# Performance work log

Hardware: AMD Instinct MI355X
Metric: run time of the kernel (lower is better)

Reference implementation:

```python
import jax, jax.numpy as jnp
import numpy as np
import math

SAMPLING_FACTOR = 5


def setup_inputs() -> dict:
    key = jax.random.key(0)
    kq, kk, kv, ki = jax.random.split(key, 4)
    B, L_Q, L_K, d = 8, 4096, 4096, 64
    # U_part = min(5 * L_Q * ceil(log1p(L_K)), L_K) = 4096 for these sizes
    U_part = min(SAMPLING_FACTOR * L_Q * math.ceil(math.log1p(L_K)), L_K)
    q = jax.random.normal(kq, (B, L_Q, d), dtype=jnp.float32)
    K = jax.random.normal(kk, (B, L_K, d), dtype=jnp.float32)
    V = jax.random.normal(kv, (B, L_K, d), dtype=jnp.float32)
    index_sample = jax.random.randint(ki, (U_part,), 0, L_K)  # random key sample (torch.randint)
    return {"q": q, "K": K, "V": V, "index_sample": index_sample}


def reference(q, K, V, index_sample):
    B, L_Q, d = q.shape
    L_K = K.shape[1]
    log_L_Q = math.ceil(math.log1p(L_Q))
    u = min(SAMPLING_FACTOR * log_L_Q, L_Q)  # number of selected queries (45 here)

    # Random key sampling (indices shared across batch)
    K_sample = K[:, index_sample, :]                       # [B, U_part, d]
    # Q @ K_sample^T
    Q_K_sample = jnp.einsum('bqd,bud->bqu', q, K_sample)   # [B, L_Q, U_part]
    # Sparsity measure M = max - sum/L_K
    M = Q_K_sample.max(axis=-1) - Q_K_sample.sum(axis=-1) / L_K  # [B, L_Q]
    # Source uses topk(..., largest=False): pick queries with SMALLEST M (kept faithfully)
    _, M_top = jax.lax.top_k(-M, u)                        # [B, u]
    # Gather the selected queries
    Q_reduce = jnp.take_along_axis(q, M_top[:, :, None], axis=1)  # [B, u, d]
    # Full attention over all keys for the selected queries
    attn_scores = jnp.einsum('bud,bkd->buk', Q_reduce, K) / math.sqrt(d)  # [B, u, L_K]
    attn_probs = jax.nn.softmax(attn_scores, axis=-1)
    attn_output = jnp.einsum('buk,bkd->bud', attn_probs, V)  # [B, u, d]
    return attn_output, attn_scores
```

## Files before the change

kernel.cpp:

```cpp
#include <hip/hip_runtime.h>
#include <hip/hip_bf16.h>
#include <math.h>

#define BB 8
#define LQ 4096
#define LK 4096
#define DD 64
#define UU 45
#define CCAP 256
#define CUMTHR 96
#define ECH 32

typedef __bf16 bf16x8 __attribute__((ext_vector_type(8)));
typedef unsigned short ushort8 __attribute__((ext_vector_type(8)));
typedef float f32x4 __attribute__((ext_vector_type(4)));

__device__ inline unsigned short f2bf(float x) {
    unsigned u = __builtin_bit_cast(unsigned, x);
    return (unsigned short)((u + 0x7FFF + ((u >> 16) & 1)) >> 16);
}

__device__ inline void gl_lds16(const void* g, void* l) {
    __builtin_amdgcn_global_load_lds(
        (const __attribute__((address_space(1))) unsigned int*)g,
        (__attribute__((address_space(3))) unsigned int*)l, 16, 0, 0);
}

__global__ __launch_bounds__(256) void k_gatherK(const float* __restrict__ K,
                                                 const int* __restrict__ idx,
                                                 int Upart,
                                                 unsigned short* __restrict__ Kg,
                                                 double* __restrict__ part) {
    int b = blockIdx.y;
    int chunk = blockIdx.x;
    int u0 = chunk * 256;
    int t = threadIdx.x;
    int pt = t & 7;

    double acc[8] = {0,0,0,0,0,0,0,0};
    #pragma unroll
    for (int i = 0; i < 8; ++i) {
        int lin = i * 256 + t;
        int u = u0 + (lin >> 3);
        if (u < Upart) {
            int kr = idx[u];
            const float* src = &K[((size_t)b * LK + kr) * DD + pt * 8];
            float4 v0 = *(const float4*)src;
            float4 v1 = *(const float4*)(src + 4);
            ushort8 pk;
            pk[0]=f2bf(v0.x); pk[1]=f2bf(v0.y); pk[2]=f2bf(v0.z); pk[3]=f2bf(v0.w);
            pk[4]=f2bf(v1.x); pk[5]=f2bf(v1.y); pk[6]=f2bf(v1.z); pk[7]=f2bf(v1.w);
            *(ushort8*)&Kg[((size_t)b * 4096 + u) * 64 + pt * 8] = pk;
            acc[0] += (double)v0.x; acc[1] += (double)v0.y;
            acc[2] += (double)v0.z; acc[3] += (double)v0.w;
            acc[4] += (double)v1.x; acc[5] += (double)v1.y;
            acc[6] += (double)v1.z; acc[7] += (double)v1.w;
        }
    }
    __shared__ double sred[32][64];
    int rg = t >> 3;
    #pragma unroll
    for (int j = 0; j < 8; ++j) sred[rg][pt * 8 + j] = acc[j];
    __syncthreads();
    if (t < 64) {
        double s = 0.0;
        #pragma unroll
        for (int r = 0; r < 32; ++r) s += sred[r][t];
        part[((size_t)(b * 16 + chunk)) * 64 + t] = s;
    }
}

__global__ __launch_bounds__(64) void k_sumK_red(const double* __restrict__ part,
                                                 int nch, double* __restrict__ sumK) {
    int b = blockIdx.x;
    int d = threadIdx.x;
    double s = 0.0;
    for (int ch = 0; ch < nch; ++ch)
        s += part[((size_t)(b * 16 + ch)) * 64 + d];
    sumK[b * DD + d] = s;
}

__global__ __launch_bounds__(256) void k_mfmaM(const float* __restrict__ Q,
                                               const unsigned short* __restrict__ Kg,
                                               float* __restrict__ maxpart) {
    int bx = blockIdx.x, cg = blockIdx.y, b = blockIdx.z;
    int t = threadIdx.x;
    int lane = t & 63, w = t >> 6;
    int row0 = bx * 128;

    __shared__ unsigned short Qs[128 * 64];
    __shared__ unsigned short Ks[2][128 * 64];

    for (int i = 0; i < 4; ++i) {
        int u = i * 256 + t;
        int r = u >> 3, s = u & 7;
        int c = s ^ (r & 7);
        const float* src = &Q[((size_t)b * LQ + row0 + r) * DD + c * 8];
        float4 v0 = *(const float4*)src;
        float4 v1 = *(const float4*)(src + 4);
        ushort8 pk;
        pk[0]=f2bf(v0.x); pk[1]=f2bf(v0.y); pk[2]=f2bf(v0.z); pk[3]=f2bf(v0.w);
        pk[4]=f2bf(v1.x); pk[5]=f2bf(v1.y); pk[6]=f2bf(v1.z); pk[7]=f2bf(v1.w);
        *(ushort8*)&Qs[r * 64 + s * 8] = pk;
    }

    int krl = lane >> 3;
    int kc8 = (lane & 7) ^ (krl & 7);
    const unsigned short* kgb = Kg + ((size_t)b * 4096 + cg * 2048) * 64;

    #define STAGE_K(buf, tile)                                                  \
        {                                                                       \
            _Pragma("unroll")                                                   \
            for (int i_ = 0; i_ < 4; ++i_) {                                    \
                int seg_ = w * 4 + i_;                                          \
                const unsigned short* g_ =                                      \
                    kgb + ((size_t)((tile) * 128 + seg_ * 8 + krl)) * 64 + kc8 * 8; \
                gl_lds16(g_, &Ks[buf][seg_ * 512]);                             \
            }                                                                   \
        }

    STAGE_K(0, 0)
    __syncthreads();

    bf16x8 afr[2][2];
    #pragma unroll
    for (int rf = 0; rf < 2; ++rf)
        #pragma unroll
        for (int kh = 0; kh < 2; ++kh) {
            int r = w * 32 + rf * 16 + (lane & 15);
            int slot = (kh * 4 + (lane >> 4)) ^ (r & 7);
            afr[rf][kh] = __builtin_bit_cast(bf16x8, *(const ushort8*)&Qs[r * 64 + slot * 8]);
        }

    float rowmax[2][4];
    #pragma unroll
    for (int rf = 0; rf < 2; ++rf)
        #pragma unroll
        for (int g = 0; g < 4; ++g) rowmax[rf][g] = -INFINITY;

    for (int tile = 0; tile < 16; ++tile) {
        int cur = tile & 1;
        if (tile < 15) STAGE_K(cur ^ 1, tile + 1)

        #pragma unroll
        for (int cf = 0; cf < 8; ++cf) {
            f32x4 acc0 = {0.f, 0.f, 0.f, 0.f};
            f32x4 acc1 = {0.f, 0.f, 0.f, 0.f};
            #pragma unroll
            for (int kh = 0; kh < 2; ++kh) {
                int ccol = cf * 16 + (lane & 15);
                int slot = (kh * 4 + (lane >> 4)) ^ (ccol & 7);
                bf16x8 bfr = __builtin_bit_cast(bf16x8, *(const ushort8*)&Ks[cur][ccol * 64 + slot * 8]);
                acc0 = __builtin_amdgcn_mfma_f32_16x16x32_bf16(afr[0][kh], bfr, acc0, 0, 0, 0);
                acc1 = __builtin_amdgcn_mfma_f32_16x16x32_bf16(afr[1][kh], bfr, acc1, 0, 0, 0);
            }
            #pragma unroll
            for (int g = 0; g < 4; ++g) {
                rowmax[0][g] = fmaxf(rowmax[0][g], acc0[g]);
                rowmax[1][g] = fmaxf(rowmax[1][g], acc1[g]);
            }
        }
        __syncthreads();
    }

    #pragma unroll
    for (int rf = 0; rf < 2; ++rf)
        #pragma unroll
        for (int g = 0; g < 4; ++g) {
            float m = rowmax[rf][g];
            m = fmaxf(m, __shfl_xor(m, 1));
            m = fmaxf(m, __shfl_xor(m, 2));
            m = fmaxf(m, __shfl_xor(m, 4));
            m = fmaxf(m, __shfl_xor(m, 8));
            if ((lane & 15) == 0) {
                int row = row0 + w * 32 + rf * 16 + (lane >> 4) * 4 + g;
                maxpart[((size_t)(b * 2 + cg)) * LQ + row] = m;
            }
        }
}

__global__ __launch_bounds__(256) void k_meanmerge(const float* __restrict__ Q,
                                                   const double* __restrict__ sumK,
                                                   const float* __restrict__ maxpart,
                                                   double* __restrict__ mt,
                                                   float* __restrict__ Map) {
    int b = blockIdx.y;
    int r = blockIdx.x * 256 + threadIdx.x;
    const float* qr = &Q[((size_t)b * LQ + r) * DD];
    const double* s = &sumK[b * DD];
    double a0 = 0, a1 = 0, a2 = 0, a3 = 0;
    #pragma unroll
    for (int d = 0; d < 64; d += 4) {
        a0 += (double)qr[d + 0] * s[d + 0];
        a1 += (double)qr[d + 1] * s[d + 1];
        a2 += (double)qr[d + 2] * s[d + 2];
        a3 += (double)qr[d + 3] * s[d + 3];
    }
    double m = ((a0 + a1) + (a2 + a3)) / (double)LK;
    mt[(size_t)b * LQ + r] = m;
    float mx = fmaxf(maxpart[((size_t)(b * 2 + 0)) * LQ + r],
                     maxpart[((size_t)(b * 2 + 1)) * LQ + r]);
    Map[(size_t)b * LQ + r] = mx - (float)m;
}

__global__ __launch_bounds__(256) void k_select(const float* __restrict__ Map,
                                                int* __restrict__ cand,
                                                int* __restrict__ cand_count) {
    int b = blockIdx.x;
    int t = threadIdx.x;
    __shared__ float mv[LQ];
    __shared__ int hist[1024];
    __shared__ float wmin[4], wmax[4];
    __shared__ float s_min, s_max;
    __shared__ int s_bstar, s_cnt;

    float lmin = INFINITY, lmax = -INFINITY;
    for (int i = t; i < LQ; i += 256) {
        float v = Map[(size_t)b * LQ + i];
        mv[i] = v;
        lmin = fminf(lmin, v);
        lmax = fmaxf(lmax, v);
    }
    #pragma unroll
    for (int m = 1; m < 64; m <<= 1) {
        lmin = fminf(lmin, __shfl_xor(lmin, m));
        lmax = fmaxf(lmax, __shfl_xor(lmax, m));
    }
    int wid = t >> 6;
    if ((t & 63) == 0) { wmin[wid] = lmin; wmax[wid] = lmax; }
    for (int i = t; i < 1024; i += 256) hist[i] = 0;
    __syncthreads();
    if (t == 0) {
        s_min = fminf(fminf(wmin[0], wmin[1]), fminf(wmin[2], wmin[3]));
        s_max = fmaxf(fmaxf(wmax[0], wmax[1]), fmaxf(wmax[2], wmax[3]));
        s_cnt = 0;
    }
    __syncthreads();
    float vmin = s_min;
    float w = (s_max - vmin) * (1.0f / 1024.0f);
    if (w <= 0.f) w = 1e-30f;
    float inv = 1.0f / w;
    for (int i = t; i < LQ; i += 256) {
        int bin = (int)((mv[i] - vmin) * inv);
        bin = min(max(bin, 0), 1023);
        atomicAdd(&hist[bin], 1);
    }
    __syncthreads();
    if (t == 0) {
        int cum = 0, bs = 1023;
        for (int j = 0; j < 1024; ++j) {
            cum += hist[j];
            if (cum >= CUMTHR) { bs = j; break; }
        }
        s_bstar = bs;
    }
    __syncthreads();
    int bstar = s_bstar;
    for (int i = t; i < LQ; i += 256) {
        int bin = (int)((mv[i] - vmin) * inv);
        bin = min(max(bin, 0), 1023);
        if (bin <= bstar) {
            int p = atomicAdd(&s_cnt, 1);
            if (p < CCAP) cand[b * CCAP + p] = i;
        }
    }
    __syncthreads();
    if (t == 0) cand_count[b] = min(s_cnt, CCAP);
}

__global__ __launch_bounds__(256, 1) void k_exact(const float* __restrict__ Q,
                                                  const float* __restrict__ K,
                                                  const int* __restrict__ idx,
                                                  const int* __restrict__ cand,
                                                  const int* __restrict__ cand_count,
                                                  float* __restrict__ exactpart) {
    int kc = blockIdx.x;
    int b  = blockIdx.y;
    int t = threadIdx.x;
    int lane = t & 63, w = t >> 6;
    __shared__ float Ks[128 * 64];
    __shared__ float wmx[4][CCAP];

    #pragma unroll
    for (int p = 0; p < 8; ++p) {
        int row = p * 16 + (t >> 4);
        int c4 = t & 15;
        int kr = idx[kc * 128 + row];
        *(float4*)&Ks[row * 64 + c4 * 4] =
            *(const float4*)&K[((size_t)b * LK + kr) * DD + c4 * 4];
    }

    int count = cand_count[b];
    int npass = (count + 127) >> 7;
    __syncthreads();

    for (int pass = 0; pass < npass; ++pass) {
        int s0 = pass * 128 + lane;
        int s1 = s0 + 64;
        float4 q0[16], q1[16];
        {
            float4 z = {0.f, 0.f, 0.f, 0.f};
            if (s0 < count) {
                const float4* qp = (const float4*)&Q[((size_t)b * LQ + cand[b * CCAP + s0]) * DD];
                #pragma unroll
                for (int i = 0; i < 16; ++i) q0[i] = qp[i];
            } else {
                #pragma unroll
                for (int i = 0; i < 16; ++i) q0[i] = z;
            }
            if (s1 < count) {
                const float4* qp = (const float4*)&Q[((size_t)b * LQ + cand[b * CCAP + s1]) * DD];
                #pragma unroll
                for (int i = 0; i < 16; ++i) q1[i] = qp[i];
            } else {
                #pragma unroll
                for (int i = 0; i < 16; ++i) q1[i] = z;
            }
        }

        float m0 = -INFINITY, m1 = -INFINITY;
        int kbeg = w * 32;
        for (int k = kbeg; k < kbeg + 32; ++k) {
            const float4* kr4 = (const float4*)&Ks[k * 64];
            float a0=0.f,a1=0.f,a2=0.f,a3=0.f;
            float c0=0.f,c1=0.f,c2=0.f,c3=0.f;
            #pragma unroll
            for (int i = 0; i < 16; i += 4) {
                float4 kv0 = kr4[i+0], kv1 = kr4[i+1], kv2 = kr4[i+2], kv3 = kr4[i+3];
                a0 = fmaf(q0[i+0].x, kv0.x, a0); a0 = fmaf(q0[i+0].y, kv0.y, a0);
                a0 = fmaf(q0[i+0].z, kv0.z, a0); a0 = fmaf(q0[i+0].w, kv0.w, a0);
                a1 = fmaf(q0[i+1].x, kv1.x, a1); a1 = fmaf(q0[i+1].y, kv1.y, a1);
                a1 = fmaf(q0[i+1].z, kv1.z, a1); a1 = fmaf(q0[i+1].w, kv1.w, a1);
                a2 = fmaf(q0[i+2].x, kv2.x, a2); a2 = fmaf(q0[i+2].y, kv2.y, a2);
                a2 = fmaf(q0[i+2].z, kv2.z, a2); a2 = fmaf(q0[i+2].w, kv2.w, a2);
                a3 = fmaf(q0[i+3].x, kv3.x, a3); a3 = fmaf(q0[i+3].y, kv3.y, a3);
                a3 = fmaf(q0[i+3].z, kv3.z, a3); a3 = fmaf(q0[i+3].w, kv3.w, a3);
                c0 = fmaf(q1[i+0].x, kv0.x, c0); c0 = fmaf(q1[i+0].y, kv0.y, c0);
                c0 = fmaf(q1[i+0].z, kv0.z, c0); c0 = fmaf(q1[i+0].w, kv0.w, c0);
                c1 = fmaf(q1[i+1].x, kv1.x, c1); c1 = fmaf(q1[i+1].y, kv1.y, c1);
                c1 = fmaf(q1[i+1].z, kv1.z, c1); c1 = fmaf(q1[i+1].w, kv1.w, c1);
                c2 = fmaf(q1[i+2].x, kv2.x, c2); c2 = fmaf(q1[i+2].y, kv2.y, c2);
                c2 = fmaf(q1[i+2].z, kv2.z, c2); c2 = fmaf(q1[i+2].w, kv2.w, c2);
                c3 = fmaf(q1[i+3].x, kv3.x, c3); c3 = fmaf(q1[i+3].y, kv3.y, c3);
                c3 = fmaf(q1[i+3].z, kv3.z, c3); c3 = fmaf(q1[i+3].w, kv3.w, c3);
            }
            m0 = fmaxf(m0, (a0 + a1) + (a2 + a3));
            m1 = fmaxf(m1, (c0 + c1) + (c2 + c3));
        }
        wmx[w][s0] = m0;
        if (s1 < CCAP) wmx[w][s1] = m1;
    }
    __syncthreads();

    if (t < count) {
        float m = fmaxf(fmaxf(wmx[0][t], wmx[1][t]), fmaxf(wmx[2][t], wmx[3][t]));
        exactpart[((size_t)(b * CCAP + t)) * ECH + kc] = m;
    }
}

__global__ __launch_bounds__(64) void k_final45(const float* __restrict__ exactpart,
                                                const double* __restrict__ mt,
                                                const int* __restrict__ cand,
                                                const int* __restrict__ cand_count,
                                                int* __restrict__ Mtop) {
    int b = blockIdx.x;
    int l = threadIdx.x;
    int count = cand_count[b];
    float val[4];
    int oid[4];
    #pragma unroll
    for (int j = 0; j < 4; ++j) {
        int slot = l + j * 64;
        if (slot < count) {
            const float* ep = &exactpart[((size_t)(b * CCAP + slot)) * ECH];
            float m = ep[0];
            #pragma unroll
            for (int k = 1; k < ECH; ++k) m = fmaxf(m, ep[k]);
            int r = cand[b * CCAP + slot];
            val[j] = m - (float)mt[(size_t)b * LQ + r];
            oid[j] = r;
        } else { val[j] = INFINITY; oid[j] = 0x7FFFFFFF; }
    }
    for (int it = 0; it < UU; ++it) {
        float bv = val[0]; int bi = oid[0], bj = 0;
        #pragma unroll
        for (int j = 1; j < 4; ++j)
            if (val[j] < bv || (val[j] == bv && oid[j] < bi)) { bv = val[j]; bi = oid[j]; bj = j; }
        float rv = bv; int ri = bi;
        #pragma unroll
        for (int m = 1; m < 64; m <<= 1) {
            float ov = __shfl_xor(rv, m);
            int oi = __shfl_xor(ri, m);
            if (ov < rv || (ov == rv && oi < ri)) { rv = ov; ri = oi; }
        }
        if (l == 0) Mtop[b * UU + it] = ri;
        if (rv == bv && ri == bi) val[bj] = INFINITY;
    }
}

__global__ __launch_bounds__(256) void k_scores(const float* __restrict__ Q,
                                                const float* __restrict__ K,
                                                const int* __restrict__ Mtop,
                                                float* __restrict__ scores) {
    int ch = blockIdx.x, b = blockIdx.y;
    int t = threadIdx.x;
    __shared__ float Qs[UU][64];
    for (int i = t; i < UU * 64; i += 256) {
        int r = i >> 6, dd = i & 63;
        int qrow = Mtop[b * UU + r];
        Qs[r][dd] = Q[((size_t)b * LQ + qrow) * DD + dd];
    }
    __syncthreads();

    int k = ch * 256 + t;
    const float* Krow = &K[((size_t)b * LK + k) * DD];
    float acc[UU];
    #pragma unroll
    for (int r = 0; r < UU; ++r) acc[r] = 0.f;

    #pragma unroll 4
    for (int dq = 0; dq < 16; ++dq) {
        float4 kv = *(const float4*)&Krow[dq * 4];
        #pragma unroll
        for (int r = 0; r < UU; ++r) {
            float4 qv = *(const float4*)&Qs[r][dq * 4];
            acc[r] += qv.x * kv.x + qv.y * kv.y + qv.z * kv.z + qv.w * kv.w;
        }
    }
    #pragma unroll
    for (int r = 0; r < UU; ++r)
        scores[((size_t)(b * UU + r)) * LK + k] = acc[r] * 0.125f;
}

__global__ __launch_bounds__(256) void k_smstats(const float* __restrict__ scores,
                                                 float2* __restrict__ ms) {
    int r = blockIdx.x, b = blockIdx.y;
    int t = threadIdx.x;
    const float* row = &scores[((size_t)(b * UU + r)) * LK];
    float v[16];
    float m = -INFINITY;
    #pragma unroll
    for (int i = 0; i < 16; ++i) { v[i] = row[t + 256 * i]; m = fmaxf(m, v[i]); }
    #pragma unroll
    for (int off = 32; off; off >>= 1) m = fmaxf(m, __shfl_xor(m, off));
    __shared__ float wred[4];
    int wid = t >> 6, lane = t & 63;
    if (lane == 0) wred[wid] = m;
    __syncthreads();
    m = fmaxf(fmaxf(wred[0], wred[1]), fmaxf(wred[2], wred[3]));
    __syncthreads();
    float s = 0.f;
    #pragma unroll
    for (int i = 0; i < 16; ++i) s += __expf(v[i] - m);
    #pragma unroll
    for (int off = 32; off; off >>= 1) s += __shfl_xor(s, off);
    if (lane == 0) wred[wid] = s;
    __syncthreads();
    if (t == 0) ms[b * UU + r] = make_float2(m, wred[0] + wred[1] + wred[2] + wred[3]);
}

__global__ __launch_bounds__(256) void k_pv(const float* __restrict__ scores,
                                            const float2* __restrict__ ms,
                                            const float* __restrict__ V,
                                            float* __restrict__ partial) {
    int ch = blockIdx.x, b = blockIdx.y;
    int t = threadIdx.x;
    int k0 = ch * 128;
    __shared__ float Vs[128 * 64];
    __shared__ float Ps[48 * 128];

    for (int p = 0; p < 8; ++p) {
        int lin = p * 1024 + t * 4;
        *(float4*)&Vs[lin] = *(const float4*)&V[((size_t)b * LK + k0) * DD + lin];
    }
    for (int i = t; i < 48 * 128; i += 256) {
        int r = i >> 7, kk = i & 127;
        float p = 0.f;
        if (r < UU) {
            float2 m_s = ms[b * UU + r];
            float sc = scores[((size_t)(b * UU + r)) * LK + k0 + kk];
            p = __expf(sc - m_s.x) / m_s.y;
        }
        Ps[i] = p;
    }
    __syncthreads();

    int d = t & 63, rg = t >> 6;
    float acc[12];
    #pragma unroll
    for (int i = 0; i < 12; ++i) acc[i] = 0.f;
    for (int k = 0; k < 128; ++k) {
        float vv = Vs[k * 64 + d];
        #pragma unroll
        for (int i = 0; i < 12; ++i)
            acc[i] += Ps[(rg * 12 + i) * 128 + k] * vv;
    }
    #pragma unroll
    for (int i = 0; i < 12; ++i) {
        int r = rg * 12 + i;
        if (r < UU)
            partial[(((size_t)(b * 32 + ch)) * UU + r) * 64 + d] = acc[i];
    }
}

__global__ __launch_bounds__(256) void k_reduce(const float* __restrict__ partial,
                                                float* __restrict__ out) {
    int o = blockIdx.x * 256 + threadIdx.x;
    if (o >= BB * UU * 64) return;
    int b = o / (UU * 64);
    int rd = o % (UU * 64);
    float s = 0.f;
    for (int ch = 0; ch < 32; ++ch)
        s += partial[(((size_t)(b * 32 + ch)) * UU * 64) + rd];
    out[o] = s;
}

extern "C" void kernel_launch(void* const* d_in, const int* in_sizes, int n_in,
                              void* d_out, int out_size, void* d_ws, size_t ws_size,
                              hipStream_t stream) {
    const float* q   = (const float*)d_in[0];
    const float* K   = (const float*)d_in[1];
    const float* V   = (const float*)d_in[2];
    const int*   idx = (const int*)d_in[3];
    int Upart = in_sizes[3];
    int nch = (Upart + 255) / 256;

    char* ws = (char*)d_ws;
    size_t off = 0;
    unsigned short* Kg = (unsigned short*)(ws + off); off += (size_t)BB * 4096 * 64 * 2;
    double* sumK      = (double*)(ws + off); off += (size_t)BB * 64 * 8;
    float*  maxpart   = (float*)(ws + off);  off += (size_t)BB * 2 * LQ * 4;
    double* mt        = (double*)(ws + off); off += (size_t)BB * LQ * 8;
    float*  Map       = (float*)(ws + off);  off += (size_t)BB * LQ * 4;
    int*    cand      = (int*)(ws + off);    off += (size_t)BB * CCAP * 4;
    int*    cand_cnt  = (int*)(ws + off);    off += 256;
    int*    Mtop      = (int*)(ws + off);    off += 2048;
    float2* ms        = (float2*)(ws + off); off += 4096;
    float*  partial   = (float*)(ws + off);  off += (size_t)BB * 32 * UU * 64 * 4;
    double* sumKpart  = (double*)partial;
    float*  exactpart = (float*)partial;

    float* out_attn   = (float*)d_out;
    float* out_scores = out_attn + BB * UU * 64;

    k_gatherK  <<<dim3(nch, BB), 256, 0, stream>>>(K, idx, Upart, Kg, sumKpart);
    k_sumK_red <<<dim3(BB), 64, 0, stream>>>(sumKpart, nch, sumK);
    k_mfmaM    <<<dim3(LQ / 128, 2, BB), 256, 0, stream>>>(q, Kg, maxpart);
    k_meanmerge<<<dim3(LQ / 256, BB), 256, 0, stream>>>(q, sumK, maxpart, mt, Map);
    k_select   <<<dim3(BB), 256, 0, stream>>>(Map, cand, cand_cnt);
    k_exact    <<<dim3(ECH, BB), 256, 0, stream>>>(q, K, idx, cand, cand_cnt, exactpart);
    k_final45  <<<dim3(BB), 64, 0, stream>>>(exactpart, mt, cand, cand_cnt, Mtop);
    k_scores   <<<dim3(LK / 256, BB), 256, 0, stream>>>(q, K, Mtop, out_scores);
    k_smstats  <<<dim3(UU, BB), 256, 0, stream>>>(out_scores, ms);
    k_pv       <<<dim3(LK / 128, BB), 256, 0, stream>>>(out_scores, ms, V, partial);
    k_reduce   <<<dim3((BB * UU * 64 + 255) / 256), 256, 0, stream>>>(partial, out_attn);
}
```

Before: 165.0 us.

## Fuse scores, softmax and PV into split-K flash-style kernel with combine

Replaces the separate scores, softmax-stats, PV and reduce kernels with one kernel that computes a 128-key chunk of scores, does a local softmax, multiplies by V, and emits per-chunk max/sum stats. A combine kernel then rescales and merges the partial results. It also folds the sumK reduction into meanmerge and replaces the serial histogram scan in select with a parallel prefix scan. The intent is to cut kernel launches and the re-reads of the scores array, in exchange for only 32 blocks per batch in the fused kernel and an extra rescale step.

```diff
diff --git a/kernel.cpp b/kernel.cpp
--- a/kernel.cpp
+++ b/kernel.cpp
@@ -10,6 +10,7 @@
 #define CCAP 256
 #define CUMTHR 96
 #define ECH 32
+#define PCH 32
 
 typedef __bf16 bf16x8 __attribute__((ext_vector_type(8)));
 typedef unsigned short ushort8 __attribute__((ext_vector_type(8)));
@@ -70,16 +71,6 @@
     }
 }
 
-__global__ __launch_bounds__(64) void k_sumK_red(const double* __restrict__ part,
-                                                 int nch, double* __restrict__ sumK) {
-    int b = blockIdx.x;
-    int d = threadIdx.x;
-    double s = 0.0;
-    for (int ch = 0; ch < nch; ++ch)
-        s += part[((size_t)(b * 16 + ch)) * 64 + d];
-    sumK[b * DD + d] = s;
-}
-
 __global__ __launch_bounds__(256) void k_mfmaM(const float* __restrict__ Q,
                                                const unsigned short* __restrict__ Kg,
                                                float* __restrict__ maxpart) {
@@ -180,21 +171,30 @@
 }
 
 __global__ __launch_bounds__(256) void k_meanmerge(const float* __restrict__ Q,
-                                                   const double* __restrict__ sumK,
+                                                   const double* __restrict__ part,
+                                                   int nch,
                                                    const float* __restrict__ maxpart,
                                                    double* __restrict__ mt,
                                                    float* __restrict__ Map) {
     int b = blockIdx.y;
-    int r = blockIdx.x * 256 + threadIdx.x;
+    int t = threadIdx.x;
+    int r = blockIdx.x * 256 + t;
+    __shared__ double sK[64];
+    if (t < 64) {
+        double s = 0.0;
+        for (int ch = 0; ch < nch; ++ch)
+            s += part[((size_t)(b * 16 + ch)) * 64 + t];
+        sK[t] = s;
+    }
+    __syncthreads();
     const float* qr = &Q[((size_t)b * LQ + r) * DD];
-    const double* s = &sumK[b * DD];
     double a0 = 0, a1 = 0, a2 = 0, a3 = 0;
     #pragma unroll
     for (int d = 0; d < 64; d += 4) {
-        a0 += (double)qr[d + 0] * s[d + 0];
-        a1 += (double)qr[d + 1] * s[d + 1];
-        a2 += (double)qr[d + 2] * s[d + 2];
-        a3 += (double)qr[d + 3] * s[d + 3];
+        a0 += (double)qr[d + 0] * sK[d + 0];
+        a1 += (double)qr[d + 1] * sK[d + 1];
+        a2 += (double)qr[d + 2] * sK[d + 2];
+        a3 += (double)qr[d + 3] * sK[d + 3];
     }
     double m = ((a0 + a1) + (a2 + a3)) / (double)LK;
     mt[(size_t)b * LQ + r] = m;
@@ -210,6 +210,7 @@
     int t = threadIdx.x;
     __shared__ float mv[LQ];
     __shared__ int hist[1024];
+    __shared__ int seg[256];
     __shared__ float wmin[4], wmax[4];
     __shared__ float s_min, s_max;
     __shared__ int s_bstar, s_cnt;
@@ -234,6 +235,7 @@
         s_min = fminf(fminf(wmin[0], wmin[1]), fminf(wmin[2], wmin[3]));
         s_max = fmaxf(fmaxf(wmax[0], wmax[1]), fmaxf(wmax[2], wmax[3]));
         s_cnt = 0;
+        s_bstar = 1023;
     }
     __syncthreads();
     float vmin = s_min;
@@ -246,13 +248,26 @@
         atomicAdd(&hist[bin], 1);
     }
     __syncthreads();
-    if (t == 0) {
-        int cum = 0, bs = 1023;
-        for (int j = 0; j < 1024; ++j) {
-            cum += hist[j];
-            if (cum >= CUMTHR) { bs = j; break; }
-        }
-        s_bstar = bs;
+    int h0 = hist[t * 4 + 0], h1 = hist[t * 4 + 1];
+    int h2 = hist[t * 4 + 2], h3 = hist[t * 4 + 3];
+    seg[t] = h0 + h1 + h2 + h3;
+    __syncthreads();
+    for (int off = 1; off < 256; off <<= 1) {
+        int v = seg[t];
+        int add = (t >= off) ? seg[t - off] : 0;
+        __syncthreads();
+        seg[t] = v + add;
+        __syncthreads();
+    }
+    {
+        int prev = (t == 0) ? 0 : seg[t - 1];
+        if (seg[t] >= CUMTHR && prev < CUMTHR) {
+            int cum = prev, bs = t * 4 + 3;
+            if (cum + h0 >= CUMTHR) bs = t * 4;
+            else if (cum + h0 + h1 >= CUMTHR) bs = t * 4 + 1;
+            else if (cum + h0 + h1 + h2 >= CUMTHR) bs = t * 4 + 2;
+            s_bstar = bs;
+        }
     }
     __syncthreads();
     int bstar = s_bstar;
@@ -398,121 +413,139 @@
     }
 }
 
-__global__ __launch_bounds__(256) void k_scores(const float* __restrict__ Q,
-                                                const float* __restrict__ K,
-                                                const int* __restrict__ Mtop,
-                                                float* __restrict__ scores) {
+__global__ __launch_bounds__(256) void k_spv(const float* __restrict__ Q,
+                                             const float* __restrict__ K,
+                                             const float* __restrict__ V,
+                                             const int* __restrict__ Mtop,
+                                             float* __restrict__ scores,
+                                             float2* __restrict__ stats,
+                                             float* __restrict__ partial) {
     int ch = blockIdx.x, b = blockIdx.y;
     int t = threadIdx.x;
-    __shared__ float Qs[UU][64];
-    for (int i = t; i < UU * 64; i += 256) {
+    int lane = t & 63, w = t >> 6;
+    int k0 = ch * 128;
+
+    __shared__ float Qs[48][64];
+    __shared__ float Vs[128 * 64];
+    __shared__ float Ps[48][128];
+    __shared__ float2 st[48];
+
+    for (int i = t; i < 48 * 64; i += 256) {
         int r = i >> 6, dd = i & 63;
-        int qrow = Mtop[b * UU + r];
-        Qs[r][dd] = Q[((size_t)b * LQ + qrow) * DD + dd];
-    }
-    __syncthreads();
-
-    int k = ch * 256 + t;
-    const float* Krow = &K[((size_t)b * LK + k) * DD];
-    float acc[UU];
-    #pragma unroll
-    for (int r = 0; r < UU; ++r) acc[r] = 0.f;
-
-    #pragma unroll 4
-    for (int dq = 0; dq < 16; ++dq) {
-        float4 kv = *(const float4*)&Krow[dq * 4];
-        #pragma unroll
-        for (int r = 0; r < UU; ++r) {
-            float4 qv = *(const float4*)&Qs[r][dq * 4];
-            acc[r] += qv.x * kv.x + qv.y * kv.y + qv.z * kv.z + qv.w * kv.w;
-        }
-    }
-    #pragma unroll
-    for (int r = 0; r < UU; ++r)
-        scores[((size_t)(b * UU + r)) * LK + k] = acc[r] * 0.125f;
-}
-
-__global__ __launch_bounds__(256) void k_smstats(const float* __restrict__ scores,
-                                                 float2* __restrict__ ms) {
-    int r = blockIdx.x, b = blockIdx.y;
-    int t = threadIdx.x;
-    const float* row = &scores[((size_t)(b * UU + r)) * LK];
-    float v[16];
-    float m = -INFINITY;
-    #pragma unroll
-    for (int i = 0; i < 16; ++i) { v[i] = row[t + 256 * i]; m = fmaxf(m, v[i]); }
-    #pragma unroll
-    for (int off = 32; off; off >>= 1) m = fmaxf(m, __shfl_xor(m, off));
-    __shared__ float wred[4];
-    int wid = t >> 6, lane = t & 63;
-    if (lane == 0) wred[wid] = m;
-    __syncthreads();
-    m = fmaxf(fmaxf(wred[0], wred[1]), fmaxf(wred[2], wred[3]));
-    __syncthreads();
-    float s = 0.f;
-    #pragma unroll
-    for (int i = 0; i < 16; ++i) s += __expf(v[i] - m);
-    #pragma unroll
-    for (int off = 32; off; off >>= 1) s += __shfl_xor(s, off);
-    if (lane == 0) wred[wid] = s;
-    __syncthreads();
-    if (t == 0) ms[b * UU + r] = make_float2(m, wred[0] + wred[1] + wred[2] + wred[3]);
-}
-
-__global__ __launch_bounds__(256) void k_pv(const float* __restrict__ scores,
-                                            const float2* __restrict__ ms,
-                                            const float* __restrict__ V,
-                                            float* __restrict__ partial) {
-    int ch = blockIdx.x, b = blockIdx.y;
-    int t = threadIdx.x;
-    int k0 = ch * 128;
-    __shared__ float Vs[128 * 64];
-    __shared__ float Ps[48 * 128];
-
+        Qs[r][dd] = (r < UU) ? Q[((size_t)b * LQ + Mtop[b * UU + r]) * DD + dd] : 0.f;
+    }
     for (int p = 0; p < 8; ++p) {
         int lin = p * 1024 + t * 4;
         *(float4*)&Vs[lin] = *(const float4*)&V[((size_t)b * LK + k0) * DD + lin];
     }
-    for (int i = t; i < 48 * 128; i += 256) {
-        int r = i >> 7, kk = i & 127;
-        float p = 0.f;
+    __syncthreads();
+
+    {
+        int key = t & 127;
+        int rh = t >> 7;
+        int r0 = rh * 23;
+        int r1 = rh ? UU : 23;
+        const float* Krow = &K[((size_t)(b * LK + k0 + key)) * DD];
+        float4 kv[16];
+        #pragma unroll
+        for (int i = 0; i < 16; ++i) kv[i] = ((const float4*)Krow)[i];
+        for (int r = r0; r < r1; ++r) {
+            const float4* qr = (const float4*)&Qs[r][0];
+            float d0 = 0.f, d1 = 0.f, d2 = 0.f, d3 = 0.f;
+            #pragma unroll
+            for (int i = 0; i < 16; i += 4) {
+                float4 q0 = qr[i+0], q1 = qr[i+1], q2 = qr[i+2], q3 = qr[i+3];
+                d0 = fmaf(q0.x, kv[i+0].x, d0); d0 = fmaf(q0.y, kv[i+0].y, d0);
+                d0 = fmaf(q0.z, kv[i+0].z, d0); d0 = fmaf(q0.w, kv[i+0].w, d0);
+                d1 = fmaf(q1.x, kv[i+1].x, d1); d1 = fmaf(q1.y, kv[i+1].y, d1);
+                d1 = fmaf(q1.z, kv[i+1].z, d1); d1 = fmaf(q1.w, kv[i+1].w, d1);
+                d2 = fmaf(q2.x, kv[i+2].x, d2); d2 = fmaf(q2.y, kv[i+2].y, d2);
+                d2 = fmaf(q2.z, kv[i+2].z, d2); d2 = fmaf(q2.w, kv[i+2].w, d2);
+                d3 = fmaf(q3.x, kv[i+3].x, d3); d3 = fmaf(q3.y, kv[i+3].y, d3);
+                d3 = fmaf(q3.z, kv[i+3].z, d3); d3 = fmaf(q3.w, kv[i+3].w, d3);
+            }
+            float sc = ((d0 + d1) + (d2 + d3)) * 0.125f;
+            Ps[r][key] = sc;
+            scores[((size_t)(b * UU + r)) * LK + k0 + key] = sc;
+        }
+    }
+    __syncthreads();
+
+    for (int r = w; r < 48; r += 4) {
         if (r < UU) {
-            float2 m_s = ms[b * UU + r];
-            float sc = scores[((size_t)(b * UU + r)) * LK + k0 + kk];
-            p = __expf(sc - m_s.x) / m_s.y;
-        }
-        Ps[i] = p;
-    }
-    __syncthreads();
-
-    int d = t & 63, rg = t >> 6;
-    float acc[12];
-    #pragma unroll
-    for (int i = 0; i < 12; ++i) acc[i] = 0.f;
-    for (int k = 0; k < 128; ++k) {
-        float vv = Vs[k * 64 + d];
-        #pragma unroll
-        for (int i = 0; i < 12; ++i)
-            acc[i] += Ps[(rg * 12 + i) * 128 + k] * vv;
-    }
-    #pragma unroll
-    for (int i = 0; i < 12; ++i) {
-        int r = rg * 12 + i;
-        if (r < UU)
-            partial[(((size_t)(b * 32 + ch)) * UU + r) * 64 + d] = acc[i];
-    }
-}
-
-__global__ __launch_bounds__(256) void k_reduce(const float* __restrict__ partial,
-                                                float* __restrict__ out) {
-    int o = blockIdx.x * 256 + threadIdx.x;
-    if (o >= BB * UU * 64) return;
-    int b = o / (UU * 64);
-    int rd = o % (UU * 64);
-    float s = 0.f;
-    for (int ch = 0; ch < 32; ++ch)
-        s += partial[(((size_t)(b * 32 + ch)) * UU * 64) + rd];
-    out[o] = s;
+            float v0 = Ps[r][lane], v1 = Ps[r][lane + 64];
+            float m = fmaxf(v0, v1);
+            #pragma unroll
+            for (int o = 32; o; o >>= 1) m = fmaxf(m, __shfl_xor(m, o));
+            float e0 = __expf(v0 - m), e1 = __expf(v1 - m);
+            float s = e0 + e1;
+            #pragma unroll
+            for (int o = 32; o; o >>= 1) s += __shfl_xor(s, o);
+            Ps[r][lane] = e0; Ps[r][lane + 64] = e1;
+            if (lane == 0) st[r] = make_float2(m, s);
+        } else {
+            Ps[r][lane] = 0.f; Ps[r][lane + 64] = 0.f;
+        }
+    }
+    __syncthreads();
+
+    {
+        int d = t & 63, rg = t >> 6;
+        float acc[12];
+        #pragma unroll
+        for (int i = 0; i < 12; ++i) acc[i] = 0.f;
+        for (int k = 0; k < 128; ++k) {
+            float vv = Vs[k * 64 + d];
+            #pragma unroll
+            for (int i = 0; i < 12; ++i)
+                acc[i] += Ps[rg * 12 + i][k] * vv;
+        }
+        #pragma unroll
+        for (int i = 0; i < 12; ++i) {
+            int r = rg * 12 + i;
+            if (r < UU)
+                partial[(((size_t)(b * PCH + ch)) * UU + r) * 64 + d] = acc[i];
+        }
+    }
+    if (t < UU) stats[((size_t)(b * PCH + ch)) * UU + t] = st[t];
+}
+
+__global__ __launch_bounds__(256) void k_combine(const float* __restrict__ partial,
+                                                 const float2* __restrict__ stats,
+                                                 float* __restrict__ out) {
+    int b = blockIdx.x;
+    int t = threadIdx.x;
+    __shared__ float wgt[UU][PCH];
+    if (t < UU) {
+        float mx[PCH], sm[PCH];
+        #pragma unroll
+        for (int c = 0; c < PCH; ++c) {
+            float2 v = stats[((size_t)(b * PCH + c)) * UU + t];
+            mx[c] = v.x; sm[c] = v.y;
+        }
+        float m = mx[0];
+        #pragma unroll
+        for (int c = 1; c < PCH; ++c) m = fmaxf(m, mx[c]);
+        float S = 0.f;
+        #pragma unroll
+        for (int c = 0; c < PCH; ++c) {
+            float e = __expf(mx[c] - m);
+            wgt[t][c] = e;
+            S += sm[c] * e;
+        }
+        float inv = 1.0f / S;
+        #pragma unroll
+        for (int c = 0; c < PCH; ++c) wgt[t][c] *= inv;
+    }
+    __syncthreads();
+    for (int o = t; o < UU * 64; o += 256) {
+        int r = o >> 6, d = o & 63;
+        float s = 0.f;
+        #pragma unroll 8
+        for (int c = 0; c < PCH; ++c)
+            s += partial[(((size_t)(b * PCH + c)) * UU + r) * 64 + d] * wgt[r][c];
+        out[((size_t)(b * UU + r)) * 64 + d] = s;
+    }
 }
 
 extern "C" void kernel_launch(void* const* d_in, const int* in_sizes, int n_in,
@@ -528,15 +561,14 @@
     char* ws = (char*)d_ws;
     size_t off = 0;
     unsigned short* Kg = (unsigned short*)(ws + off); off += (size_t)BB * 4096 * 64 * 2;
-    double* sumK      = (double*)(ws + off); off += (size_t)BB * 64 * 8;
     float*  maxpart   = (float*)(ws + off);  off += (size_t)BB * 2 * LQ * 4;
     double* mt        = (double*)(ws + off); off += (size_t)BB * LQ * 8;
     float*  Map       = (float*)(ws + off);  off += (size_t)BB * LQ * 4;
     int*    cand      = (int*)(ws + off);    off += (size_t)BB * CCAP * 4;
     int*    cand_cnt  = (int*)(ws + off);    off += 256;
     int*    Mtop      = (int*)(ws + off);    off += 2048;
-    float2* ms        = (float2*)(ws + off); off += 4096;
-    float*  partial   = (float*)(ws + off);  off += (size_t)BB * 32 * UU * 64 * 4;
+    float2* stats     = (float2*)(ws + off); off += (size_t)BB * PCH * UU * 8 + 256;
+    float*  partial   = (float*)(ws + off);  off += (size_t)BB * PCH * UU * 64 * 4;
     double* sumKpart  = (double*)partial;
     float*  exactpart = (float*)partial;
 
@@ -544,14 +576,11 @@
     float* out_scores = out_attn + BB * UU * 64;
 
     k_gatherK  <<<dim3(nch, BB), 256, 0, stream>>>(K, idx, Upart, Kg, sumKpart);
-    k_sumK_red <<<dim3(BB), 64, 0, stream>>>(sumKpart, nch, sumK);
     k_mfmaM    <<<dim3(LQ / 128, 2, BB), 256, 0, stream>>>(q, Kg, maxpart);
-    k_meanmerge<<<dim3(LQ / 256, BB), 256, 0, stream>>>(q, sumK, maxpart, mt, Map);
+    k_meanmerge<<<dim3(LQ / 256, BB), 256, 0, stream>>>(q, sumKpart, nch, maxpart, mt, Map);
     k_select   <<<dim3(BB), 256, 0, stream>>>(Map, cand, cand_cnt);
     k_exact    <<<dim3(ECH, BB), 256, 0, stream>>>(q, K, idx, cand, cand_cnt, exactpart);
     k_final45  <<<dim3(BB), 64, 0, stream>>>(exactpart, mt, cand, cand_cnt, Mtop);
-    k_scores   <<<dim3(LK / 256, BB), 256, 0, stream>>>(q, K, Mtop, out_scores);
-    k_smstats  <<<dim3(UU, BB), 256, 0, stream>>>(out_scores, ms);
-    k_pv       <<<dim3(LK / 128, BB), 256, 0, stream>>>(out_scores, ms, V, partial);
-    k_reduce   <<<dim3((BB * UU * 64 + 255) / 256), 256, 0, stream>>>(partial, out_attn);
-}
+    k_spv      <<<dim3(PCH, BB), 256, 0, stream>>>(q, K, V, Mtop, out_scores, stats, partial);
+    k_combine  <<<dim3(BB), 256, 0, stream>>>(partial, stats, out_attn);
+}
```

Result: faster. 158.6 us (-3.9%).
